# Performance work log

Measured on AMD Instinct MI355X. Metric: run time of the kernel, lower is better.

## Reference

```python
import jax, jax.numpy as jnp
import numpy as np

B, Q, N_WAY, K_SHOT = 2, 75, 5, 5
C, H, W = 640, 5, 5
PROJ, HEAD_DIM = 640, 32
NUM_HEAD = PROJ // HEAD_DIM
SCALE = HEAD_DIM ** 0.5
TEMP = 12.5
ALPHAS = [2.0 ** k for k in range(-3, 2)]  # cfg.model.mmd.alphas**k, k in [-3,2)


def setup_inputs() -> dict:
    key = jax.random.key(0)
    ks = jax.random.split(key, 7)
    std = (2.0 / PROJ) ** 0.5  # torch init: normal(0, sqrt(2/(k*k*out)))
    return {
        "support_xf": jax.random.normal(ks[0], (B, N_WAY * K_SHOT, C, H, W), jnp.float32),
        "support_y": jax.random.randint(ks[1], (B, N_WAY * K_SHOT), 0, N_WAY),
        "query_xf": jax.random.normal(ks[2], (B, Q, C, H, W), jnp.float32),
        "query_y": jax.random.randint(ks[3], (B, Q), 0, N_WAY),
        "Wq": jax.random.normal(ks[4], (PROJ, C), jnp.float32) * std,
        "Wk": jax.random.normal(ks[5], (PROJ, C), jnp.float32) * std,
        "Wv": jax.random.normal(ks[6], (C, C), jnp.float32) * ((2.0 / C) ** 0.5),
    }


def _qkv(x, Wq, Wk, Wv):
    # x: [b, n, c, h, w]; 1x1 convs == channel matmuls
    b, n, c, h, w = x.shape
    xf = x.reshape(b, n, c, h * w)
    proj = lambda Wm: jnp.einsum('oc,bncp->bnop', Wm, xf)
    k = proj(Wk).reshape(b, n, NUM_HEAD, -1, h * w)                   # [b,n,nh,hd,p]
    q = proj(Wq).reshape(b, n, NUM_HEAD, -1, h * w).swapaxes(-1, -2)  # [b,n,nh,p,hd]
    v = proj(Wv).reshape(b, n, NUM_HEAD, -1, h * w).swapaxes(-1, -2)  # [b,n,nh,p,ch]
    return q, k, v


def _cross_attn(q, k, v, shortcut, dim):
    # q:[b,*,*,nh,p,hd], k:[b,*,*,nh,hd,p], v:[b,*,*,nh,p,ch] (broadcasting over q/s axes)
    attn = jax.nn.softmax((q / SCALE) @ k, axis=-1)
    out = attn @ v                                  # [b,Q,S,nh,p,ch]
    b, nq, s = out.shape[:3]
    h, w = shortcut.shape[-2:]
    out = out.swapaxes(-1, -2).reshape(b, nq, s, -1, h, w)  # [b,Q,S,c,h,w]
    return out + jnp.expand_dims(shortcut, dim)


def _sqdist(x, y):
    # squared euclidean pairwise distances over last-two dims; == cdist(x,y)**2
    xx = jnp.sum(x * x, -1)[..., :, None]
    yy = jnp.sum(y * y, -1)[..., None, :]
    d2 = xx + yy - 2.0 * jnp.einsum('...nc,...mc->...nm', x, y)
    return jnp.maximum(d2, 0.0)


def _mgk(d2):
    # multi-scale gaussian kernel: sum_a exp(-a * dist^2)
    k = jnp.exp(-ALPHAS[0] * d2)
    for a in ALPHAS[1:]:
        k = k + jnp.exp(-a * d2)
    return k


def _forward(support_xf, query_xf, query_y, Wq, Wk, Wv):
    b, q, c, h, w = query_xf.shape
    sq, sk, sv = _qkv(support_xf, Wq, Wk, Wv)
    qq_, qk_, qv_ = _qkv(query_xf, Wq, Wk, Wv)
    # support features attended by query queries (shortcut = support, broadcast over q)
    sbq = _cross_attn(qq_[:, :, None], sk[:, None], sv[:, None], support_xf, dim=1)  # [b,q,s,c,h,w]
    # query features attended by support queries (shortcut = query, broadcast over s)
    qbs = _cross_attn(sq[:, None], qk_[:, :, None], qv_[:, :, None], query_xf, dim=2)

    def regroup(t):  # [b,q,s,c,h,w] -> [b,q,n_way,k_shot*h*w,c]
        t = t.reshape(b, q, N_WAY, K_SHOT, c, h, w)
        return t.transpose(0, 1, 2, 3, 5, 6, 4).reshape(b, q, N_WAY, K_SHOT * h * w, c)

    sxf = regroup(sbq)
    qxf = regroup(qbs)
    # centering over channel dim
    sxf = sxf - sxf.mean(-1, keepdims=True)
    qxf = qxf - qxf.mean(-1, keepdims=True)

    Kss = _mgk(_sqdist(sxf, sxf))  # [b,q,n_way,N,N]
    Kqq = _mgk(_sqdist(qxf, qxf))
    Kqs = _mgk(_sqdist(sxf, qxf))

    N = K_SHOT * h * w  # num features per class-group (== num_fea_per_img)
    tot = lambda K: jnp.sum(K, (-1, -2))
    tr = lambda K: jnp.trace(K, axis1=-2, axis2=-1)  # diagonal removal (::N+1 stride)
    mmd = (tot(Kss) - tr(Kss)) / (N * (N - 1)) \
        + (tot(Kqq) - tr(Kqq)) / (N * (N - 1)) \
        - (2.0 / (N * N)) * tot(Kqs)
    mmd_dis = mmd.reshape(b * q, N_WAY)

    logp = jax.nn.log_softmax(-mmd_dis / TEMP, axis=-1)
    y = query_y.reshape(-1)
    loss = -jnp.mean(jnp.take_along_axis(logp, y[:, None], axis=1))
    return loss


def reference(support_xf, support_y, query_xf, query_y, Wq, Wk, Wv):
    return _forward(support_xf, query_xf, query_y, Wq, Wk, Wv)
```

## Files before the change

### kernel.cpp

```cpp
#include <hip/hip_runtime.h>
#include <math.h>

#define PP    25
#define CCH   640
#define NCOL  5000
#define SCALE_INV 0.17677669529663687f

#define XTB_OFF   0L
#define WB_OFF    1600000L
#define PROJB_OFF 2214400L
#define MMD_OFF   7014400L
#define ONES_OFF  7015168L
#define FEAT_OFF  7015360L
#define FEAT_PER_WAY_US 160000L
#define FEAT_PER_PAIR_US 800000L

typedef __attribute__((ext_vector_type(8)))  short          s16x8;
typedef __attribute__((ext_vector_type(8)))  unsigned short u16x8;
typedef __attribute__((ext_vector_type(4)))  unsigned short u16x4;
typedef __attribute__((ext_vector_type(16))) float          f32x16;

typedef __attribute__((address_space(1))) const unsigned int glb_u32;
typedef __attribute__((address_space(3))) unsigned int       lds_u32;

__device__ inline unsigned short f2bf(float x) {
  unsigned u = __float_as_uint(x);
  unsigned r = u + 0x7fff + ((u >> 16) & 1);
  return (unsigned short)(r >> 16);
}
__device__ inline float bf2f(unsigned short b) {
  return __uint_as_float(((unsigned)b) << 16);
}
__device__ inline unsigned cvtpk(float lo, float hi) {
  unsigned r;
  asm("v_cvt_pk_bf16_f32 %0, %1, %2" : "=v"(r) : "v"(lo), "v"(hi));
  return r;
}
__device__ inline void plswap(unsigned &a, unsigned &b) {
  asm volatile("v_permlane32_swap_b32 %0, %1" : "+v"(a), "+v"(b));
}

__global__ __launch_bounds__(256) void t_kernel(const float* __restrict__ sup,
                                                const float* __restrict__ qry,
                                                unsigned short* __restrict__ XTB) {
  __shared__ float lds[16000];
  int item = blockIdx.x;
  const float* src = (item < 50) ? (sup + item * 16000) : (qry + (item - 50) * 16000);
  int tid = threadIdx.x;
  for (int e = tid * 4; e < 16000; e += 1024)
    *(float4*)&lds[e] = *(const float4*)&src[e];
  __syncthreads();
  int ibase = item * PP;
  for (int e = tid * 4; e < 16000; e += 1024) {
    int p = e / CCH, c = e - p * CCH;
    u16x4 b;
    b.x = f2bf(lds[(c + 0) * PP + p]);
    b.y = f2bf(lds[(c + 1) * PP + p]);
    b.z = f2bf(lds[(c + 2) * PP + p]);
    b.w = f2bf(lds[(c + 3) * PP + p]);
    *(u16x4*)&XTB[(long)(ibase + p) * CCH + c] = b;
  }
}

__global__ __launch_bounds__(256) void w_kernel(const float* __restrict__ Wq,
                                                const float* __restrict__ Wk,
                                                const float* __restrict__ Wv,
                                                unsigned short* __restrict__ WB,
                                                unsigned short* __restrict__ ones) {
  if (blockIdx.x == 0 && threadIdx.x < 384)
    ones[threadIdx.x] = (threadIdx.x < 64) ? (unsigned short)0x3F80 : (unsigned short)0;
  long base = ((long)blockIdx.x * 256 + threadIdx.x) * 8;
  int m = (int)(base / 409600L);
  long off = base - (long)m * 409600L;
  const float* W = (m == 0) ? Wq : ((m == 1) ? Wk : Wv);
  float4 a = *(const float4*)&W[off];
  float4 c = *(const float4*)&W[off + 4];
  u16x8 v;
  v[0] = f2bf(a.x); v[1] = f2bf(a.y); v[2] = f2bf(a.z); v[3] = f2bf(a.w);
  v[4] = f2bf(c.x); v[5] = f2bf(c.y); v[6] = f2bf(c.z); v[7] = f2bf(c.w);
  *(u16x8*)&WB[base] = v;
}

__global__ __launch_bounds__(512) void proj_kernel(const unsigned short* __restrict__ WB,
                                                   const unsigned short* __restrict__ XTB,
                                                   unsigned short* __restrict__ proj) {
  __shared__ __align__(16) unsigned short At[128 * 64];
  __shared__ __align__(16) unsigned short Bt[128 * 64];
  int m = blockIdx.z;
  int ctile = blockIdx.x * 128, otile = blockIdx.y * 128;
  const unsigned short* Wsrc = WB + (long)m * 409600L;
  unsigned short* out = proj + (long)m * NCOL * CCH;
  int tid = threadIdx.x;
  int w = tid >> 6, lane = tid & 63;
  int wr = w >> 2, wc = w & 3;
  int lr = lane & 31, ksel = lane >> 5;
  int sr = tid >> 2, sg = (tid & 3) * 2;

  f32x16 acc[2];
#pragma unroll
  for (int a = 0; a < 2; a++)
#pragma unroll
    for (int e = 0; e < 16; e++) acc[a][e] = 0.f;

  int bcol = ctile + sr;
  const unsigned short* asrc = Wsrc + (long)(otile + sr) * CCH + sg * 8;
  const unsigned short* bsrc = XTB + (long)bcol * CCH + sg * 8;

  u16x8 pa[2], pb[2];
#pragma unroll
  for (int gi = 0; gi < 2; gi++) {
    pa[gi] = *(const u16x8*)&asrc[gi * 8];
    if (bcol < NCOL) pb[gi] = *(const u16x8*)&bsrc[gi * 8];
    else { u16x8 z; for (int e = 0; e < 8; e++) z[e] = 0; pb[gi] = z; }
  }

  for (int kc = 0; kc < 10; kc++) {
    __syncthreads();
#pragma unroll
    for (int gi = 0; gi < 2; gi++) {
      int g = sg + gi;
      *(u16x8*)&At[sr * 64 + ((g ^ (sr & 7)) << 3)] = pa[gi];
      *(u16x8*)&Bt[sr * 64 + ((g ^ (sr & 7)) << 3)] = pb[gi];
    }
    if (kc < 9) {
      const unsigned short* an = asrc + (kc + 1) * 64;
      const unsigned short* bn = bsrc + (kc + 1) * 64;
#pragma unroll
      for (int gi = 0; gi < 2; gi++) {
        pa[gi] = *(const u16x8*)&an[gi * 8];
        if (bcol < NCOL) pb[gi] = *(const u16x8*)&bn[gi * 8];
      }
    }
    __syncthreads();
#pragma unroll
    for (int ks = 0; ks < 4; ks++) {
      int gk = ks * 2 + ksel;
      s16x8 bf1;
      {
        int R = wc * 32 + lr;
        bf1 = *(const s16x8*)&Bt[R * 64 + ((gk ^ (R & 7)) << 3)];
      }
#pragma unroll
      for (int a = 0; a < 2; a++) {
        int R = (wr + 2 * a) * 32 + lr;
        s16x8 af = *(const s16x8*)&At[R * 64 + ((gk ^ (R & 7)) << 3)];
        acc[a] = __builtin_amdgcn_mfma_f32_32x32x16_bf16(af, bf1, acc[a], 0, 0, 0);
      }
    }
  }

  int col = ctile + wc * 32 + lr;
  if (col < NCOL) {
#pragma unroll
    for (int a = 0; a < 2; a++) {
      int obase = otile + (wr + 2 * a) * 32 + 4 * ksel;
#pragma unroll
      for (int g2 = 0; g2 < 4; g2++) {
        u16x4 v;
        v.x = f2bf(acc[a][g2 * 4 + 0]);
        v.y = f2bf(acc[a][g2 * 4 + 1]);
        v.z = f2bf(acc[a][g2 * 4 + 2]);
        v.w = f2bf(acc[a][g2 * 4 + 3]);
        *(u16x4*)&out[(long)col * CCH + obase + g2 * 8] = v;
      }
    }
  }
}

template<int SIDE>
__global__ __launch_bounds__(256) void attn_kernel(const unsigned short* __restrict__ proj,
                                                   const unsigned short* __restrict__ XTB,
                                                   unsigned short* __restrict__ feat,
                                                   int chunk_start) {
  int tid = threadIdx.x, wid = tid >> 6, lane = tid & 63;
  int lr = lane & 31, hf = lane >> 5;
  int rclamp = lr > 24 ? 24 : lr;
  int bid = blockIdx.x;
  int pw = bid / 5, grp = bid - pw * 5;
  int head = grp * 4 + wid;
  int lpi = pw / 5, way = pw - lpi * 5;
  int pair = chunk_start + lpi;
  int b = pair / 75;
  int qitem = 50 + pair;
  int qcol = qitem * PP;
  int sitem0 = b * 25 + way * 5;
  int ho = head * 32;
  const unsigned short* Qp = proj;
  const unsigned short* Kp = proj + (long)NCOL * CCH;
  const unsigned short* Vp = proj + 2L * NCOL * CCH;
  unsigned short* fb = feat + (long)pw * FEAT_PER_WAY_US + head * 250 * 32;

  auto ldfrag = [&](const unsigned short* src, int col0, int ks) -> s16x8 {
    return *(const s16x8*)&src[(long)(col0 + rclamp) * CCH + ho + ks * 16 + hf * 8];
  };
  auto ldvfrag = [&](int col0, int ks) -> s16x8 {
    const unsigned short* base = Vp + (long)(col0 + ks * 16 + hf * 8) * CCH + ho + lr;
    s16x8 f;
#pragma unroll
    for (int j = 0; j < 8; j++) f[j] = (short)base[(long)j * CCH];
    return f;
  };

  s16x8 fA0, fA1, fB0, fB1, fV0, fV1;
  float scv[16];
  if (SIDE == 0) {
    fB0 = ldfrag(Qp, qcol, 0); fB1 = ldfrag(Qp, qcol, 1);
  } else {
    fA0 = ldfrag(Kp, qcol, 0); fA1 = ldfrag(Kp, qcol, 1);
    fV0 = ldvfrag(qcol, 0);    fV1 = ldvfrag(qcol, 1);
#pragma unroll
    for (int rg = 0; rg < 16; rg++) {
      int q = (rg & 3) + 8 * (rg >> 2) + 4 * hf;
      int qc = q > 24 ? 24 : q;
      scv[rg] = bf2f(XTB[(long)(qcol + qc) * CCH + ho + lr]);
    }
  }

#pragma unroll
  for (int shot = 0; shot < 5; shot++) {
    int scol = (sitem0 + shot) * PP;
    s16x8 A0, A1, B0, B1, V0, V1;
    if (SIDE == 0) {
      A0 = ldfrag(Kp, scol, 0); A1 = ldfrag(Kp, scol, 1);
      B0 = fB0; B1 = fB1;
      V0 = ldvfrag(scol, 0);    V1 = ldvfrag(scol, 1);
    } else {
      A0 = fA0; A1 = fA1;
      B0 = ldfrag(Qp, scol, 0); B1 = ldfrag(Qp, scol, 1);
      V0 = fV0; V1 = fV1;
    }
    f32x16 s;
#pragma unroll
    for (int e = 0; e < 16; e++) s[e] = 0.f;
    s = __builtin_amdgcn_mfma_f32_32x32x16_bf16(A0, B0, s, 0, 0, 0);
    s = __builtin_amdgcn_mfma_f32_32x32x16_bf16(A1, B1, s, 0, 0, 0);
    float t8[8];
#pragma unroll
    for (int i = 0; i < 8; i++) t8[i] = fmaxf(s[i], s[i + 8]);
#pragma unroll
    for (int i = 0; i < 4; i++) t8[i] = fmaxf(t8[i], t8[i + 4]);
    float mx = fmaxf(fmaxf(t8[0], t8[1]), fmaxf(t8[2], t8[3]));
    mx = fmaxf(mx, __shfl_xor(mx, 32));
    float pv[16];
#pragma unroll
    for (int rg = 0; rg < 16; rg++) pv[rg] = __expf((s[rg] - mx) * SCALE_INV);
    pv[13] = 0.f; pv[14] = 0.f; pv[15] = 0.f;
    if (hf) pv[12] = 0.f;
    float s8[8];
#pragma unroll
    for (int i = 0; i < 8; i++) s8[i] = pv[i] + pv[i + 8];
#pragma unroll
    for (int i = 0; i < 4; i++) s8[i] = s8[i] + s8[i + 4];
    float sum = (s8[0] + s8[1]) + (s8[2] + s8[3]);
    sum += __shfl_xor(sum, 32);
    float rinv = 1.f / sum;
    union { unsigned u[4]; s16x8 v; } P0u, P1u;
    {
      unsigned a0 = cvtpk(pv[0], pv[1]),  a1 = cvtpk(pv[2], pv[3]);
      unsigned a2 = cvtpk(pv[4], pv[5]),  a3 = cvtpk(pv[6], pv[7]);
      plswap(a2, a0);
      plswap(a3, a1);
      P0u.u[0] = a0; P0u.u[1] = a1; P0u.u[2] = a2; P0u.u[3] = a3;
      unsigned b0 = cvtpk(pv[8], pv[9]),   b1 = cvtpk(pv[10], pv[11]);
      unsigned b2 = cvtpk(pv[12], pv[13]), b3 = cvtpk(pv[14], pv[15]);
      plswap(b2, b0);
      plswap(b3, b1);
      P1u.u[0] = b0; P1u.u[1] = b1; P1u.u[2] = b2; P1u.u[3] = b3;
    }
    f32x16 o;
#pragma unroll
    for (int e = 0; e < 16; e++) o[e] = 0.f;
    o = __builtin_amdgcn_mfma_f32_32x32x16_bf16(P0u.v, V0, o, 0, 0, 0);
    o = __builtin_amdgcn_mfma_f32_32x32x16_bf16(P1u.v, V1, o, 0, 0, 0);
    unsigned short* frow = fb + (long)((SIDE ? 125 : 0) + shot * 25) * 32;
    const unsigned short* scb = XTB + (long)(scol + 4 * hf) * CCH + ho + lr;
#pragma unroll
    for (int i = 0; i < 8; i++) {
      int rg0 = 2 * i, rg1 = rg0 + 1;
      int qoff = (rg0 & 3) + 8 * (rg0 >> 2);
      int q0 = qoff + 4 * hf, q1 = q0 + 1;
      float sc0, sc1;
      if (SIDE) { sc0 = scv[rg0]; sc1 = scv[rg1]; }
      else {
        sc0 = bf2f(scb[(long)qoff * CCH]);
        sc1 = bf2f(scb[(long)(qoff + 1) * CCH]);
      }
      unsigned u = cvtpk(fmaf(o[rg0], rinv, sc0), fmaf(o[rg1], rinv, sc1));
      if (q0 < 25) frow[q0 * 32 + lr] = (unsigned short)u;
      if (q1 < 25) frow[q1 * 32 + lr] = (unsigned short)(u >> 16);
    }
  }
}

__global__ __launch_bounds__(1024) void gram_kernel(const unsigned short* __restrict__ feat,
                                                    const unsigned short* __restrict__ ones,
                                                    float* __restrict__ mmd,
                                                    int chunk_start) {
  __shared__ __align__(16) unsigned short tile[2][16384];
  __shared__ float sums[256], nrmsq[256], meanv[256], nrmv[256];
  __shared__ float red[48];
  int bid = blockIdx.x;
  const unsigned short* fb = feat + (long)bid * FEAT_PER_WAY_US;
  int tid = threadIdx.x;
  int w = tid >> 6, lane = tid & 63;
  int wr = w >> 2, wc = w & 3;
  int lr = lane & 31, ksel = lane >> 5;

  const unsigned short* srcp[2];
  long stepv[2];
#pragma unroll
  for (int i = 0; i < 2; i++) {
    int s = (w * 2 + i) * 64 + lane;
    int row = s >> 3, gs = s & 7, g = gs ^ (row & 7);
    if (row < 250) {
      srcp[i] = fb + (long)((g >> 2) * 250 + row) * 32 + (g & 3) * 8;
      stepv[i] = 16000;
    } else {
      srcp[i] = ones + (row - 250) * 64 + g * 8;
      stepv[i] = 0;
    }
  }

  f32x16 acc[2][2];
#pragma unroll
  for (int a = 0; a < 2; a++)
#pragma unroll
    for (int b2 = 0; b2 < 2; b2++)
#pragma unroll
      for (int e = 0; e < 16; e++) acc[a][b2][e] = 0.f;

#pragma unroll
  for (int i = 0; i < 2; i++)
    __builtin_amdgcn_global_load_lds((glb_u32*)srcp[i],
                                     (lds_u32*)&tile[0][(w * 2 + i) * 512], 16, 0, 0);
  __syncthreads();

  for (int kc = 0; kc < 10; kc++) {
    int cur = kc & 1;
    if (kc < 9) {
#pragma unroll
      for (int i = 0; i < 2; i++)
        __builtin_amdgcn_global_load_lds((glb_u32*)(srcp[i] + (long)(kc + 1) * stepv[i]),
                                         (lds_u32*)&tile[cur ^ 1][(w * 2 + i) * 512], 16, 0, 0);
    }
    const unsigned short* tb = tile[cur];
#pragma unroll
    for (int ks = 0; ks < 4; ks++) {
      int gk = ks * 2 + ksel;
      s16x8 af[2], bfv[2];
#pragma unroll
      for (int a = 0; a < 2; a++) {
        int R = (wr + 4 * a) * 32 + lr;
        af[a] = *(const s16x8*)&tb[R * 64 + ((gk ^ (R & 7)) << 3)];
      }
#pragma unroll
      for (int b2 = 0; b2 < 2; b2++) {
        int R = (wc + 4 * b2) * 32 + lr;
        bfv[b2] = *(const s16x8*)&tb[R * 64 + ((gk ^ (R & 7)) << 3)];
      }
#pragma unroll
      for (int a = 0; a < 2; a++)
#pragma unroll
        for (int b2 = 0; b2 < 2; b2++)
          acc[a][b2] = __builtin_amdgcn_mfma_f32_32x32x16_bf16(af[a], bfv[b2], acc[a][b2], 0, 0, 0);
    }
    __syncthreads();
  }

#pragma unroll
  for (int a = 0; a < 2; a++) {
    int ti = wr + 4 * a;
#pragma unroll
    for (int b2 = 0; b2 < 2; b2++) {
      int tj = wc + 4 * b2;
      int col = tj * 32 + lr;
      if (col == 250) {
#pragma unroll
        for (int rg = 0; rg < 16; rg++) {
          int row = ti * 32 + (rg & 3) + 8 * (rg >> 2) + 4 * ksel;
          if (row < 250) sums[row] = acc[a][b2][rg];
        }
      }
      if (ti == tj) {
#pragma unroll
        for (int rg = 0; rg < 16; rg++) {
          int row = ti * 32 + (rg & 3) + 8 * (rg >> 2) + 4 * ksel;
          if (row == col && row < 250) nrmsq[row] = acc[a][b2][rg];
        }
      }
    }
  }
  __syncthreads();
  if (tid < 250) {
    float s0 = sums[tid];
    float m = s0 * (1.f / 640.f);
    meanv[tid] = m;
    nrmv[tid] = nrmsq[tid] - s0 * m;
  }
  __syncthreads();

  float s_ss = 0.f, s_qq = 0.f, s_x = 0.f;
#pragma unroll
  for (int a = 0; a < 2; a++) {
    int ti = wr + 4 * a;
#pragma unroll
    for (int b2 = 0; b2 < 2; b2++) {
      int tj = wc + 4 * b2;
      int col = tj * 32 + lr;
#pragma unroll
      for (int rg = 0; rg < 16; rg++) {
        int row = ti * 32 + (rg & 3) + 8 * (rg >> 2) + 4 * ksel;
        if (row < 250 && col < 250) {
          float d2 = nrmv[row] + nrmv[col] - 2.f * acc[a][b2][rg]
                   + 1280.f * meanv[row] * meanv[col];
          d2 = fmaxf(d2, 0.f);
          float e = __expf(-0.125f * d2);
          float e2 = e * e, e4 = e2 * e2, e8 = e4 * e4, e16 = e8 * e8;
          float kv = e + e2 + e4 + e8 + e16;
          bool rs = row < 125, cs = col < 125;
          if (rs && cs)        { if (row != col) s_ss += kv; }
          else if (!rs && !cs) { if (row != col) s_qq += kv; }
          else                 s_x += kv;
        }
      }
    }
  }
#pragma unroll
  for (int off = 32; off; off >>= 1) {
    s_ss += __shfl_xor(s_ss, off);
    s_qq += __shfl_xor(s_qq, off);
    s_x  += __shfl_xor(s_x, off);
  }
  if (lane == 0) { red[w * 3] = s_ss; red[w * 3 + 1] = s_qq; red[w * 3 + 2] = s_x; }
  __syncthreads();
  if (tid == 0) {
    float a = 0.f, b2 = 0.f, c = 0.f;
    for (int i = 0; i < 16; i++) { a += red[i * 3]; b2 += red[i * 3 + 1]; c += red[i * 3 + 2]; }
    mmd[(long)chunk_start * 5 + bid] = a * (1.f / 15500.f) + b2 * (1.f / 15500.f) - c * (1.f / 15625.f);
  }
}

__global__ __launch_bounds__(256) void loss_kernel(const float* __restrict__ mmd,
                                                   const int* __restrict__ qy,
                                                   float* __restrict__ out) {
  __shared__ float red[256];
  int tid = threadIdx.x;
  float val = 0.f;
  if (tid < 150) {
    float l[5];
    float mx = -1e30f;
#pragma unroll
    for (int w = 0; w < 5; w++) {
      l[w] = -mmd[tid * 5 + w] * (1.0f / 12.5f);
      mx = fmaxf(mx, l[w]);
    }
    float sum = 0.f;
#pragma unroll
    for (int w = 0; w < 5; w++) sum += __expf(l[w] - mx);
    float lse = mx + logf(sum);
    int y = qy[tid];
    val = -(l[y] - lse);
  }
  red[tid] = val;
  __syncthreads();
  for (int s = 128; s > 0; s >>= 1) {
    if (tid < s) red[tid] += red[tid + s];
    __syncthreads();
  }
  if (tid == 0) out[0] = red[0] * (1.0f / 150.0f);
}

extern "C" void kernel_launch(void* const* d_in, const int* in_sizes, int n_in,
                              void* d_out, int out_size, void* d_ws, size_t ws_size,
                              hipStream_t stream) {
  (void)in_sizes; (void)n_in; (void)out_size;
  const float* sup = (const float*)d_in[0];
  const float* qry = (const float*)d_in[2];
  const int* qy = (const int*)d_in[3];
  const float* Wq = (const float*)d_in[4];
  const float* Wk = (const float*)d_in[5];
  const float* Wv = (const float*)d_in[6];
  float* ws = (float*)d_ws;
  unsigned short* XTB = (unsigned short*)(ws + XTB_OFF);
  unsigned short* WB = (unsigned short*)(ws + WB_OFF);
  unsigned short* projB = (unsigned short*)(ws + PROJB_OFF);
  float* mmd = ws + MMD_OFF;
  unsigned short* ones = (unsigned short*)(ws + ONES_OFF);
  unsigned short* feat = (unsigned short*)(ws + FEAT_OFF);
  float* out = (float*)d_out;

  long wsf = (long)(ws_size / 4);
  long avail_us = (wsf - FEAT_OFF) * 2;
  long chunkL = avail_us / FEAT_PER_PAIR_US;
  int chunk = (chunkL > 150) ? 150 : (chunkL < 1 ? 1 : (int)chunkL);

  hipLaunchKernelGGL(t_kernel, dim3(200), dim3(256), 0, stream, sup, qry, XTB);
  hipLaunchKernelGGL(w_kernel, dim3(600), dim3(256), 0, stream, Wq, Wk, Wv, WB, ones);
  hipLaunchKernelGGL(proj_kernel, dim3(40, 5, 3), dim3(512), 0, stream, WB, XTB, projB);
  for (int c0 = 0; c0 < 150; c0 += chunk) {
    int cp = (150 - c0 < chunk) ? (150 - c0) : chunk;
    hipLaunchKernelGGL((attn_kernel<0>), dim3(cp * 25), dim3(256), 0, stream, projB, XTB, feat, c0);
    hipLaunchKernelGGL((attn_kernel<1>), dim3(cp * 25), dim3(256), 0, stream, projB, XTB, feat, c0);
    hipLaunchKernelGGL(gram_kernel, dim3(cp * 5), dim3(1024), 0, stream, feat, ones, mmd, c0);
  }
  hipLaunchKernelGGL(loss_kernel, dim3(1), dim3(256), 0, stream, mmd, qy, out);
}
```

Before: 232.3 us.

## Exploit Gram matrix symmetry: compute only upper-triangular super-tiles with 10 waves

The gram kernel now assigns its waves only to the upper-triangular 64x64 super-tiles of the symmetric 256x256 Gram matrix (10 waves instead of 16) and doubles the contribution of off-diagonal super-tiles in the kernel sums. The block shrinks from 1024 to 640 threads, and the LDS tile loads are redistributed over the smaller block. This is meant to cut MFMA and exp work by roughly a third. The cost is fewer threads per block for loading and lower per-block parallelism.

```diff
diff --git a/kernel.cpp b/kernel.cpp
--- a/kernel.cpp
+++ b/kernel.cpp
@@ -292,32 +292,39 @@
   }
 }
 
-__global__ __launch_bounds__(1024) void gram_kernel(const unsigned short* __restrict__ feat,
-                                                    const unsigned short* __restrict__ ones,
-                                                    float* __restrict__ mmd,
-                                                    int chunk_start) {
+__global__ __launch_bounds__(640) void gram_kernel(const unsigned short* __restrict__ feat,
+                                                   const unsigned short* __restrict__ ones,
+                                                   float* __restrict__ mmd,
+                                                   int chunk_start) {
   __shared__ __align__(16) unsigned short tile[2][16384];
   __shared__ float sums[256], nrmsq[256], meanv[256], nrmv[256];
-  __shared__ float red[48];
+  __shared__ float red[30];
   int bid = blockIdx.x;
   const unsigned short* fb = feat + (long)bid * FEAT_PER_WAY_US;
   int tid = threadIdx.x;
   int w = tid >> 6, lane = tid & 63;
-  int wr = w >> 2, wc = w & 3;
   int lr = lane & 31, ksel = lane >> 5;
 
-  const unsigned short* srcp[2];
-  long stepv[2];
-#pragma unroll
-  for (int i = 0; i < 2; i++) {
-    int s = (w * 2 + i) * 64 + lane;
-    int row = s >> 3, gs = s & 7, g = gs ^ (row & 7);
-    if (row < 250) {
-      srcp[i] = fb + (long)((g >> 2) * 250 + row) * 32 + (g & 3) * 8;
-      stepv[i] = 16000;
-    } else {
-      srcp[i] = ones + (row - 250) * 64 + g * 8;
-      stepv[i] = 0;
+  int sti, stj;
+  if (w < 4)      { sti = 0; stj = w; }
+  else if (w < 7) { sti = 1; stj = w - 3; }
+  else if (w < 9) { sti = 2; stj = w - 5; }
+  else            { sti = 3; stj = 3; }
+
+  const unsigned short* srcp[4];
+  long stepv[4];
+#pragma unroll
+  for (int i = 0; i < 4; i++) {
+    int s = tid + i * 640;
+    if (s < 2048) {
+      int row = s >> 3, gs = s & 7, g = gs ^ (row & 7);
+      if (row < 250) {
+        srcp[i] = fb + (long)((g >> 2) * 250 + row) * 32 + (g & 3) * 8;
+        stepv[i] = 16000;
+      } else {
+        srcp[i] = ones + (row - 250) * 64 + g * 8;
+        stepv[i] = 0;
+      }
     }
   }
 
@@ -330,18 +337,24 @@
       for (int e = 0; e < 16; e++) acc[a][b2][e] = 0.f;
 
 #pragma unroll
-  for (int i = 0; i < 2; i++)
-    __builtin_amdgcn_global_load_lds((glb_u32*)srcp[i],
-                                     (lds_u32*)&tile[0][(w * 2 + i) * 512], 16, 0, 0);
+  for (int i = 0; i < 4; i++) {
+    int s = tid + i * 640;
+    if (s < 2048)
+      __builtin_amdgcn_global_load_lds((glb_u32*)srcp[i],
+                                       (lds_u32*)&tile[0][s * 8], 16, 0, 0);
+  }
   __syncthreads();
 
   for (int kc = 0; kc < 10; kc++) {
     int cur = kc & 1;
     if (kc < 9) {
 #pragma unroll
-      for (int i = 0; i < 2; i++)
-        __builtin_amdgcn_global_load_lds((glb_u32*)(srcp[i] + (long)(kc + 1) * stepv[i]),
-                                         (lds_u32*)&tile[cur ^ 1][(w * 2 + i) * 512], 16, 0, 0);
+      for (int i = 0; i < 4; i++) {
+        int s = tid + i * 640;
+        if (s < 2048)
+          __builtin_amdgcn_global_load_lds((glb_u32*)(srcp[i] + (long)(kc + 1) * stepv[i]),
+                                           (lds_u32*)&tile[cur ^ 1][s * 8], 16, 0, 0);
+      }
     }
     const unsigned short* tb = tile[cur];
 #pragma unroll
@@ -350,12 +363,12 @@
       s16x8 af[2], bfv[2];
 #pragma unroll
       for (int a = 0; a < 2; a++) {
-        int R = (wr + 4 * a) * 32 + lr;
+        int R = (sti * 2 + a) * 32 + lr;
         af[a] = *(const s16x8*)&tb[R * 64 + ((gk ^ (R & 7)) << 3)];
       }
 #pragma unroll
       for (int b2 = 0; b2 < 2; b2++) {
-        int R = (wc + 4 * b2) * 32 + lr;
+        int R = (stj * 2 + b2) * 32 + lr;
         bfv[b2] = *(const s16x8*)&tb[R * 64 + ((gk ^ (R & 7)) << 3)];
       }
 #pragma unroll
@@ -369,10 +382,10 @@
 
 #pragma unroll
   for (int a = 0; a < 2; a++) {
-    int ti = wr + 4 * a;
+    int ti = sti * 2 + a;
 #pragma unroll
     for (int b2 = 0; b2 < 2; b2++) {
-      int tj = wc + 4 * b2;
+      int tj = stj * 2 + b2;
       int col = tj * 32 + lr;
       if (col == 250) {
 #pragma unroll
@@ -402,10 +415,12 @@
   float s_ss = 0.f, s_qq = 0.f, s_x = 0.f;
 #pragma unroll
   for (int a = 0; a < 2; a++) {
-    int ti = wr + 4 * a;
+    int ti = sti * 2 + a;
 #pragma unroll
     for (int b2 = 0; b2 < 2; b2++) {
-      int tj = wc + 4 * b2;
+      int tj = stj * 2 + b2;
+      if (ti > tj) continue;
+      float w2 = (ti < tj) ? 2.f : 1.f;
       int col = tj * 32 + lr;
 #pragma unroll
       for (int rg = 0; rg < 16; rg++) {
@@ -416,7 +431,7 @@
           d2 = fmaxf(d2, 0.f);
           float e = __expf(-0.125f * d2);
           float e2 = e * e, e4 = e2 * e2, e8 = e4 * e4, e16 = e8 * e8;
-          float kv = e + e2 + e4 + e8 + e16;
+          float kv = w2 * (e + e2 + e4 + e8 + e16);
           bool rs = row < 125, cs = col < 125;
           if (rs && cs)        { if (row != col) s_ss += kv; }
           else if (!rs && !cs) { if (row != col) s_qq += kv; }
@@ -435,7 +450,7 @@
   __syncthreads();
   if (tid == 0) {
     float a = 0.f, b2 = 0.f, c = 0.f;
-    for (int i = 0; i < 16; i++) { a += red[i * 3]; b2 += red[i * 3 + 1]; c += red[i * 3 + 2]; }
+    for (int i = 0; i < 10; i++) { a += red[i * 3]; b2 += red[i * 3 + 1]; c += red[i * 3 + 2]; }
     mmd[(long)chunk_start * 5 + bid] = a * (1.f / 15500.f) + b2 * (1.f / 15500.f) - c * (1.f / 15625.f);
   }
 }
@@ -501,7 +516,7 @@
     int cp = (150 - c0 < chunk) ? (150 - c0) : chunk;
     hipLaunchKernelGGL((attn_kernel<0>), dim3(cp * 25), dim3(256), 0, stream, projB, XTB, feat, c0);
     hipLaunchKernelGGL((attn_kernel<1>), dim3(cp * 25), dim3(256), 0, stream, projB, XTB, feat, c0);
-    hipLaunchKernelGGL(gram_kernel, dim3(cp * 5), dim3(1024), 0, stream, feat, ones, mmd, c0);
+    hipLaunchKernelGGL(gram_kernel, dim3(cp * 5), dim3(640), 0, stream, feat, ones, mmd, c0);
   }
   hipLaunchKernelGGL(loss_kernel, dim3(1), dim3(256), 0, stream, mmd, qy, out);
 }
```

Result: faster. 216.6 us (median of 3 runs) (-6.8%).

## Load gram MFMA operands directly from global memory instead of LDS tiles

Applied to the files above, without the earlier changes.

The gram kernel no longer stages feature tiles into double-buffered LDS via global_load_lds. Each wave now reads its A and B MFMA fragments straight from global memory (L1/L2), and the per-chunk barriers are gone. This frees 64KB of LDS and removes the synchronisation, but every wave re-fetches the same rows from cache, with no explicit prefetch to hide latency.

```diff
diff --git a/kernel.cpp b/kernel.cpp
--- a/kernel.cpp
+++ b/kernel.cpp
@@ -19,9 +19,6 @@
 typedef __attribute__((ext_vector_type(8)))  unsigned short u16x8;
 typedef __attribute__((ext_vector_type(4)))  unsigned short u16x4;
 typedef __attribute__((ext_vector_type(16))) float          f32x16;
-
-typedef __attribute__((address_space(1))) const unsigned int glb_u32;
-typedef __attribute__((address_space(3))) unsigned int       lds_u32;
 
 __device__ inline unsigned short f2bf(float x) {
   unsigned u = __float_as_uint(x);
@@ -296,7 +293,6 @@
                                                     const unsigned short* __restrict__ ones,
                                                     float* __restrict__ mmd,
                                                     int chunk_start) {
-  __shared__ __align__(16) unsigned short tile[2][16384];
   __shared__ float sums[256], nrmsq[256], meanv[256], nrmv[256];
   __shared__ float red[48];
   int bid = blockIdx.x;
@@ -306,19 +302,19 @@
   int wr = w >> 2, wc = w & 3;
   int lr = lane & 31, ksel = lane >> 5;
 
-  const unsigned short* srcp[2];
-  long stepv[2];
-#pragma unroll
-  for (int i = 0; i < 2; i++) {
-    int s = (w * 2 + i) * 64 + lane;
-    int row = s >> 3, gs = s & 7, g = gs ^ (row & 7);
-    if (row < 250) {
-      srcp[i] = fb + (long)((g >> 2) * 250 + row) * 32 + (g & 3) * 8;
-      stepv[i] = 16000;
-    } else {
-      srcp[i] = ones + (row - 250) * 64 + g * 8;
-      stepv[i] = 0;
-    }
+  const unsigned short* abase[2]; long ahs[2];
+  const unsigned short* bbase[2]; long bhs[2];
+#pragma unroll
+  for (int a = 0; a < 2; a++) {
+    int R = (wr + 4 * a) * 32 + lr;
+    if (R < 250) { abase[a] = fb + (long)R * 32; ahs[a] = 8000; }
+    else         { abase[a] = ones + (R - 250) * 64; ahs[a] = 0; }
+  }
+#pragma unroll
+  for (int b2 = 0; b2 < 2; b2++) {
+    int R = (wc + 4 * b2) * 32 + lr;
+    if (R < 250) { bbase[b2] = fb + (long)R * 32; bhs[b2] = 8000; }
+    else         { bbase[b2] = ones + (R - 250) * 64; bhs[b2] = 0; }
   }
 
   f32x16 acc[2][2];
@@ -329,42 +325,25 @@
 #pragma unroll
       for (int e = 0; e < 16; e++) acc[a][b2][e] = 0.f;
 
-#pragma unroll
-  for (int i = 0; i < 2; i++)
-    __builtin_amdgcn_global_load_lds((glb_u32*)srcp[i],
-                                     (lds_u32*)&tile[0][(w * 2 + i) * 512], 16, 0, 0);
-  __syncthreads();
-
   for (int kc = 0; kc < 10; kc++) {
-    int cur = kc & 1;
-    if (kc < 9) {
-#pragma unroll
-      for (int i = 0; i < 2; i++)
-        __builtin_amdgcn_global_load_lds((glb_u32*)(srcp[i] + (long)(kc + 1) * stepv[i]),
-                                         (lds_u32*)&tile[cur ^ 1][(w * 2 + i) * 512], 16, 0, 0);
-    }
-    const unsigned short* tb = tile[cur];
 #pragma unroll
     for (int ks = 0; ks < 4; ks++) {
       int gk = ks * 2 + ksel;
+      int hd = kc * 2 + (gk >> 2);
+      int co = (gk & 3) * 8;
       s16x8 af[2], bfv[2];
 #pragma unroll
-      for (int a = 0; a < 2; a++) {
-        int R = (wr + 4 * a) * 32 + lr;
-        af[a] = *(const s16x8*)&tb[R * 64 + ((gk ^ (R & 7)) << 3)];
-      }
-#pragma unroll
-      for (int b2 = 0; b2 < 2; b2++) {
-        int R = (wc + 4 * b2) * 32 + lr;
-        bfv[b2] = *(const s16x8*)&tb[R * 64 + ((gk ^ (R & 7)) << 3)];
-      }
+      for (int a = 0; a < 2; a++)
+        af[a] = *(const s16x8*)(abase[a] + hd * ahs[a] + co);
+#pragma unroll
+      for (int b2 = 0; b2 < 2; b2++)
+        bfv[b2] = *(const s16x8*)(bbase[b2] + hd * bhs[b2] + co);
 #pragma unroll
       for (int a = 0; a < 2; a++)
 #pragma unroll
         for (int b2 = 0; b2 < 2; b2++)
           acc[a][b2] = __builtin_amdgcn_mfma_f32_32x32x16_bf16(af[a], bfv[b2], acc[a][b2], 0, 0, 0);
     }
-    __syncthreads();
   }
 
 #pragma unroll
```

Measured after the change: 279.0 us. +20.1%, slower.
